# Optimization experiments

Measured on AMD Instinct MI355X. Metric: run time of the kernel, lower is better.

## Reference

```python
import jax, jax.numpy as jnp
import numpy as np

B, S, H = 1, 2048, 2048
NH, KVH = 32, 8
HD = H // NH
GROUPS = NH // KVH
ROPE_THETA = 10000.0


def _rope(x):
    # x: (b, s, heads, head_dim); HF-style rotate-half RoPE
    d = x.shape[-1]
    s = x.shape[1]
    inv_freq = 1.0 / (ROPE_THETA ** (jnp.arange(0, d, 2, dtype=jnp.float32) / d))
    t = jnp.arange(s, dtype=jnp.float32)
    freqs = jnp.einsum('s,f->sf', t, inv_freq)          # (s, d/2)
    emb = jnp.concatenate([freqs, freqs], axis=-1)       # (s, d)
    cos = jnp.cos(emb)[None, :, None, :].astype(x.dtype)
    sin = jnp.sin(emb)[None, :, None, :].astype(x.dtype)
    x1, x2 = x[..., : d // 2], x[..., d // 2:]
    rot = jnp.concatenate([-x2, x1], axis=-1)
    return x * cos + rot * sin


def setup_inputs() -> dict:
    key = jax.random.key(0)
    ks = jax.random.split(key, 6)
    scale = 0.02
    hidden_states = jax.random.normal(ks[0], (B, S, H), dtype=jnp.float32)
    Wq = jax.random.normal(ks[1], (H, NH, HD), dtype=jnp.float32) * scale
    Wk = jax.random.normal(ks[2], (H, KVH, HD), dtype=jnp.float32) * scale
    Wv = jax.random.normal(ks[3], (H, KVH, HD), dtype=jnp.float32) * scale
    Wo = jax.random.normal(ks[4], (H, H), dtype=jnp.float32) * scale
    # causal additive mask (b,1,s,s): 0 on/below diagonal, large negative above
    causal = jnp.tril(jnp.ones((S, S), dtype=bool))
    attention_mask = jnp.where(causal, 0.0, -1e9).astype(jnp.float32)[None, None]
    return {"hidden_states": hidden_states, "Wq": Wq, "Wk": Wk, "Wv": Wv,
            "Wo": Wo, "attention_mask": attention_mask}


def reference(hidden_states, Wq, Wk, Wv, Wo, attention_mask):
    b, s, _ = hidden_states.shape
    q = jnp.einsum('bsh,hnd->bsnd', hidden_states, Wq)   # (b,s,NH,HD)
    k = jnp.einsum('bsh,hnd->bsnd', hidden_states, Wk)   # (b,s,KVH,HD)
    v = jnp.einsum('bsh,hnd->bsnd', hidden_states, Wv)   # (b,s,KVH,HD)
    q = _rope(q)
    k = _rope(k)
    # GQA: tile kv heads along head axis (tf.tile semantics)
    k = jnp.tile(k, (1, 1, GROUPS, 1))                   # (b,s,NH,HD)
    v = jnp.tile(v, (1, 1, GROUPS, 1))
    # scores: 'aecd,abcd->acbe' -> (b, heads, q_len, k_len)
    scores = jnp.einsum('bend,bqnd->bnqe', k, q) / jnp.sqrt(
        jnp.asarray(HD, dtype=q.dtype))
    scores = scores + attention_mask
    scores = jnp.maximum(scores, jnp.finfo(scores.dtype).min)
    probs = jax.nn.softmax(scores, axis=-1)
    attn = jnp.einsum('bnqe,bend->bqnd', probs, v)       # (b,s,NH,HD)
    attn = attn.reshape(b, s, H)
    return jnp.einsum('bsh,hd->bsd', attn, Wo)
```

## Files before the change

kernel.cpp:

```cpp
#include <hip/hip_runtime.h>
#include <stdint.h>

typedef unsigned short u16;
typedef uint32_t u32;
typedef uint64_t u64;
typedef float f32x4 __attribute__((ext_vector_type(4)));
typedef float f32x16 __attribute__((ext_vector_type(16)));
typedef __bf16 bf16x8 __attribute__((ext_vector_type(8)));

#define S_LEN 2048
#define HID 2048
#define N_HEADS 32
#define KV_HEADS 8
#define HEAD_DIM 64
#define QKV_COLS 3072
#define QSCALE 0.18033688011112042f

__device__ __forceinline__ u16 f2b(float x) {
  union { float f; uint32_t u; } c; c.f = x;
  uint32_t u = (c.u + 0x7fffu + ((c.u >> 16) & 1u)) >> 16;
  return (u16)u;
}
__device__ __forceinline__ float b2f(u16 v) {
  union { uint32_t u; float f; } c; c.u = ((uint32_t)v) << 16;
  return c.f;
}
__device__ __forceinline__ u32 pkbf(float e, float o) {
  union { float f; u32 u; } a, b; a.f = e; b.f = o;
  return __builtin_amdgcn_perm(b.u, a.u, 0x07060302u);
}

#define GLL16(gptr, lptr)                                                      \
  __builtin_amdgcn_global_load_lds(                                            \
      (__attribute__((address_space(1))) void*)(gptr),                         \
      (__attribute__((address_space(3))) void*)(lptr), 16, 0, 0)

__global__ __launch_bounds__(256) void prep_fused(const float* __restrict__ Wq,
                                                  const float* __restrict__ Wk,
                                                  const float* __restrict__ Wv,
                                                  const float* __restrict__ Wo,
                                                  const float* __restrict__ hs,
                                                  u16* __restrict__ WqkvT,
                                                  u16* __restrict__ WoT,
                                                  u16* __restrict__ X) {
  const int b = blockIdx.x;
  const int t = threadIdx.x;
  if (b < 10240) {
    __shared__ float tile[32][33];
    const float* in;
    u16* out;
    int C, bx, by;
    if (b < 4096) { in = Wq; out = WqkvT; C = 2048; bx = b & 63; by = b >> 6; }
    else if (b < 5120) { int bb = b - 4096; in = Wk; out = WqkvT + 2048 * 2048; C = 512; bx = bb & 15; by = bb >> 4; }
    else if (b < 6144) { int bb = b - 5120; in = Wv; out = WqkvT + 2048 * 2048 + 512 * 2048; C = 512; bx = bb & 15; by = bb >> 4; }
    else { int bb = b - 6144; in = Wo; out = WoT; C = 2048; bx = bb & 63; by = bb >> 6; }
    const int tx = t & 31, ty = t >> 5;
    const int c0 = bx * 32, r0 = by * 32;
#pragma unroll
    for (int i = 0; i < 32; i += 8)
      tile[ty + i][tx] = in[(size_t)(r0 + ty + i) * C + c0 + tx];
    __syncthreads();
#pragma unroll
    for (int i = 0; i < 32; i += 8)
      out[(size_t)(c0 + ty + i) * 2048 + r0 + tx] = f2b(tile[tx][ty + i]);
  } else {
    int i = (b - 10240) * 256 + t;
    float4 v = reinterpret_cast<const float4*>(hs)[i];
    ushort4 o;
    o.x = f2b(v.x); o.y = f2b(v.y); o.z = f2b(v.z); o.w = f2b(v.w);
    reinterpret_cast<ushort4*>(X)[i] = o;
  }
}

__global__ void transpose_bf16(const u16* __restrict__ in, int istride,
                               u16* __restrict__ out, int R, int C) {
  __shared__ u16 tile[32][33];
  int c0 = blockIdx.x * 32, r0 = blockIdx.y * 32;
  int tx = threadIdx.x, ty = threadIdx.y;
#pragma unroll
  for (int i = 0; i < 32; i += 8)
    tile[ty + i][tx] = in[(size_t)(r0 + ty + i) * istride + c0 + tx];
  __syncthreads();
#pragma unroll
  for (int i = 0; i < 32; i += 8)
    out[(size_t)(c0 + ty + i) * R + r0 + tx] = tile[tx][ty + i];
}

__global__ __launch_bounds__(256) void gemm128s(const u16* __restrict__ A,
                                                const u16* __restrict__ BT,
                                                float* __restrict__ Cp,
                                                int M, int N, int K, int ksplit) {
  __shared__ __align__(16) u16 As[128 * 64];
  __shared__ __align__(16) u16 Bs[128 * 64];
  const int t = threadIdx.x;
  const int w = t >> 6, l = t & 63;
  const int lr = l & 15, lk = l >> 4;
  const int wr = w >> 1, wc = w & 1;
  const int m0 = blockIdx.x * 128, n0 = blockIdx.y * 128;
  const int z = blockIdx.z;
  const int kspan = K / ksplit;
  const int kBeg = z * kspan, kEnd = kBeg + kspan;
  Cp += (size_t)z * M * N;

  f32x4 acc[4][4];
#pragma unroll
  for (int m = 0; m < 4; ++m)
#pragma unroll
    for (int n = 0; n < 4; ++n)
      acc[m][n] = (f32x4){0.f, 0.f, 0.f, 0.f};

  const u16* aSrc = A + (size_t)(m0 + t / 8) * K + (t % 8) * 8;
  const u16* bSrc = BT + (size_t)(n0 + t / 8) * K + (t % 8) * 8;
  char* aDst = (char*)As + w * 1024;
  char* bDst = (char*)Bs + w * 1024;

  for (int k0 = kBeg; k0 < kEnd; k0 += 64) {
#pragma unroll
    for (int i = 0; i < 4; ++i)
      GLL16(aSrc + (size_t)i * 32 * K + k0, aDst + i * 4096);
#pragma unroll
    for (int i = 0; i < 4; ++i)
      GLL16(bSrc + (size_t)i * 32 * K + k0, bDst + i * 4096);
    __syncthreads();
#pragma unroll
    for (int kk = 0; kk < 2; ++kk) {
      bf16x8 af[4], bfr[4];
#pragma unroll
      for (int m = 0; m < 4; ++m)
        af[m] = *(const bf16x8*)&As[(wr * 64 + m * 16 + lr) * 64 + kk * 32 + lk * 8];
#pragma unroll
      for (int n = 0; n < 4; ++n)
        bfr[n] = *(const bf16x8*)&Bs[(wc * 64 + n * 16 + lr) * 64 + kk * 32 + lk * 8];
#pragma unroll
      for (int m = 0; m < 4; ++m)
#pragma unroll
        for (int n = 0; n < 4; ++n)
          acc[m][n] = __builtin_amdgcn_mfma_f32_16x16x32_bf16(af[m], bfr[n], acc[m][n], 0, 0, 0);
    }
    __syncthreads();
  }
#pragma unroll
  for (int m = 0; m < 4; ++m)
#pragma unroll
    for (int n = 0; n < 4; ++n) {
      int row0 = m0 + wr * 64 + m * 16 + lk * 4;
      int col = n0 + wc * 64 + n * 16 + lr;
#pragma unroll
      for (int r = 0; r < 4; ++r)
        Cp[(size_t)(row0 + r) * N + col] = acc[m][n][r];
    }
}

__global__ __launch_bounds__(256) void post_qkv(const float* __restrict__ P0,
                                                const float* __restrict__ P1,
                                                u16* __restrict__ QKV) {
  int idx = blockIdx.x * 256 + threadIdx.x;
  int s = idx / 1536, j = idx - s * 1536;
  const float* r0 = P0 + (size_t)s * QKV_COLS;
  const float* r1 = P1 + (size_t)s * QKV_COLS;
  u16* o = QKV + (size_t)s * QKV_COLS;
  if (j < 1280) {
    int hbase, i;
    float scale;
    if (j < 1024) { hbase = (j >> 5) * 64; i = j & 31; scale = QSCALE; }
    else { int jj = j - 1024; hbase = 2048 + (jj >> 5) * 64; i = jj & 31; scale = 1.0f; }
    int c1 = hbase + i, c2 = c1 + 32;
    float inv = __expf(-(float)i * (9.210340371976184f / 32.0f));
    float f = (float)s * inv;
    float sn, cs;
    sincosf(f, &sn, &cs);
    float x1 = r0[c1] + r1[c1], x2 = r0[c2] + r1[c2];
    o[c1] = f2b((x1 * cs - x2 * sn) * scale);
    o[c2] = f2b((x2 * cs + x1 * sn) * scale);
  } else {
    int c = 2560 + (j - 1280) * 2;
    *(u32*)(o + c) = pkbf(r0[c] + r1[c], r0[c + 1] + r1[c + 1]);
  }
}

__global__ __launch_bounds__(256) void post_out(const float* __restrict__ P0,
                                                const float* __restrict__ P1,
                                                float* __restrict__ out) {
  int i = blockIdx.x * 256 + threadIdx.x;
  float4 a = reinterpret_cast<const float4*>(P0)[i];
  float4 b = reinterpret_cast<const float4*>(P1)[i];
  a.x += b.x; a.y += b.y; a.z += b.z; a.w += b.w;
  reinterpret_cast<float4*>(out)[i] = a;
}

__global__ __launch_bounds__(256) void attn_kernel(const u16* __restrict__ QKV,
                                                   const u16* __restrict__ Vt,
                                                   u16* __restrict__ At) {
  __shared__ __align__(16) u16 scratch[4][32 * 64];
  const int t = threadIdx.x;
  const int w = t >> 6, l = t & 63;
  const int lq = l & 31;
  const int hi = l >> 5;
  const int b = blockIdx.x;
  const int qt = (b < 256) ? (63 - (b >> 3)) : ((b - 256) >> 3);
  const int head = (b & 7) * 4 + w;
  const int kvh = head & (KV_HEADS - 1);
  const int qbase = qt * 32;
  char* pb = (char*)scratch[w];
  const int swrow = lq * 128;
  const int swx = (lq & 7) << 4;

  bf16x8 qf[4];
  {
    const u16* qp = QKV + (size_t)(qbase + lq) * QKV_COLS + head * HEAD_DIM + hi * 8;
#pragma unroll
    for (int jj = 0; jj < 4; ++jj) qf[jj] = *(const bf16x8*)(qp + jj * 16);
  }
  const u16* Kb = QKV + HID + kvh * HEAD_DIM;
  const u16* Vb = Vt + (size_t)(kvh * HEAD_DIM) * S_LEN;

  f32x16 oacc0, oacc1;
#pragma unroll
  for (int i = 0; i < 16; ++i) { oacc0[i] = 0.f; oacc1[i] = 0.f; }
  float m_run = -1e30f;
  float l_run = 0.f;

  auto loadK = [&](int kv0, bf16x8* k0, bf16x8* k1) {
    const u16* kp = Kb + (size_t)(kv0 + lq) * QKV_COLS + hi * 8;
#pragma unroll
    for (int jj = 0; jj < 4; ++jj) {
      k0[jj] = *(const bf16x8*)(kp + jj * 16);
      k1[jj] = *(const bf16x8*)(kp + (size_t)32 * QKV_COLS + jj * 16);
    }
  };

  auto tile = [&](int kv0, const bf16x8* kf0, const bf16x8* kf1, bool mask0, bool mask1) {
    f32x16 s0, s1;
#pragma unroll
    for (int i = 0; i < 16; ++i) { s0[i] = 0.f; s1[i] = 0.f; }
#pragma unroll
    for (int jj = 0; jj < 4; ++jj)
      s0 = __builtin_amdgcn_mfma_f32_32x32x16_bf16(kf0[jj], qf[jj], s0, 0, 0, 0);
#pragma unroll
    for (int jj = 0; jj < 4; ++jj)
      s1 = __builtin_amdgcn_mfma_f32_32x32x16_bf16(kf1[jj], qf[jj], s1, 0, 0, 0);
    bf16x8 vf0[4], vf1[4];
    const u16* vp = Vb + (size_t)lq * S_LEN + kv0 + hi * 8;
#pragma unroll
    for (int ks = 0; ks < 4; ++ks) {
      vf0[ks] = *(const bf16x8*)(vp + ks * 16);
      vf1[ks] = *(const bf16x8*)(vp + (size_t)32 * S_LEN + ks * 16);
    }
    if (mask0) {
      const int c = kv0 - qbase;
#pragma unroll
      for (int r = 0; r < 16; ++r) {
        int kvr = (r & 3) + 8 * (r >> 2) + 4 * hi + c;
        s0[r] = (kvr > lq) ? -1e30f : s0[r];
      }
    }
    if (mask1) {
      const int c = kv0 + 32 - qbase;
#pragma unroll
      for (int r = 0; r < 16; ++r) {
        int kvr = (r & 3) + 8 * (r >> 2) + 4 * hi + c;
        s1[r] = (kvr > lq) ? -1e30f : s1[r];
      }
    }
    float mx[16];
#pragma unroll
    for (int r = 0; r < 16; ++r) mx[r] = fmaxf(s0[r], s1[r]);
#pragma unroll
    for (int st = 8; st >= 1; st >>= 1)
#pragma unroll
      for (int r = 0; r < st; ++r) mx[r] = fmaxf(mx[r], mx[r + st]);
    float pm = mx[0];
    pm = fmaxf(pm, __shfl_xor(pm, 32));
    if (!__all(pm <= m_run + 8.f)) {
      float mnew = fmaxf(m_run, pm);
      float esc = exp2f(m_run - mnew);
      m_run = mnew;
      l_run *= esc;
#pragma unroll
      for (int i = 0; i < 16; ++i) { oacc0[i] *= esc; oacc1[i] *= esc; }
    }
#pragma unroll
    for (int r = 0; r < 16; ++r) {
      s0[r] = exp2f(s0[r] - m_run);
      s1[r] = exp2f(s1[r] - m_run);
    }
    float ls[16];
#pragma unroll
    for (int r = 0; r < 16; ++r) ls[r] = s0[r] + s1[r];
#pragma unroll
    for (int st = 8; st >= 1; st >>= 1)
#pragma unroll
      for (int r = 0; r < st; ++r) ls[r] += ls[r + st];
    l_run += ls[0];
#pragma unroll
    for (int sb = 0; sb < 2; ++sb)
#pragma unroll
      for (int g = 0; g < 4; ++g) {
        u32 w0 = sb ? pkbf(s1[4 * g + 0], s1[4 * g + 1]) : pkbf(s0[4 * g + 0], s0[4 * g + 1]);
        u32 w1 = sb ? pkbf(s1[4 * g + 2], s1[4 * g + 3]) : pkbf(s0[4 * g + 2], s0[4 * g + 3]);
        int kvb2 = (32 * sb + 8 * g + 4 * hi) * 2;
        *(u64*)(pb + swrow + (kvb2 ^ swx)) = (u64)w0 | ((u64)w1 << 32);
      }
    asm volatile("s_waitcnt lgkmcnt(0)" ::: "memory");
    __builtin_amdgcn_sched_barrier(0);
    bf16x8 pa[4];
#pragma unroll
    for (int ks = 0; ks < 4; ++ks)
      pa[ks] = *(const bf16x8*)(pb + swrow + ((32 * ks + 16 * hi) ^ swx));
    asm volatile("" ::: "memory");
#pragma unroll
    for (int ks = 0; ks < 4; ++ks) {
      oacc0 = __builtin_amdgcn_mfma_f32_32x32x16_bf16(vf0[ks], pa[ks], oacc0, 0, 0, 0);
      oacc1 = __builtin_amdgcn_mfma_f32_32x32x16_bf16(vf1[ks], pa[ks], oacc1, 0, 0, 0);
    }
  };

  const int NTF = qt >> 1;
  bf16x8 ka0[4], ka1[4], kb0[4], kb1[4];
  loadK(0, ka0, ka1);
  int tl = 0;
  for (; tl + 2 <= NTF; tl += 2) {
    loadK((tl + 1) * 64, kb0, kb1);
    tile(tl * 64, ka0, ka1, false, false);
    loadK((tl + 2) * 64, ka0, ka1);
    tile((tl + 1) * 64, kb0, kb1, false, false);
  }
  if (tl < NTF) {
    loadK((tl + 1) * 64, kb0, kb1);
    tile(tl * 64, ka0, ka1, false, false);
    tile(NTF * 64, kb0, kb1, (qt & 1) == 0, true);
  } else {
    tile(NTF * 64, ka0, ka1, (qt & 1) == 0, true);
  }

  float l_tot = l_run + __shfl_xor(l_run, 32);
  float inv = 1.0f / l_tot;
  asm volatile("" ::: "memory");
#pragma unroll
  for (int dt = 0; dt < 2; ++dt) {
#pragma unroll
    for (int j = 0; j < 8; ++j) {
      int d = dt * 32 + 2 * (j & 1) + 8 * (j >> 1) + 4 * hi;
      float e = (dt ? oacc1[2 * j] : oacc0[2 * j]) * inv;
      float o = (dt ? oacc1[2 * j + 1] : oacc0[2 * j + 1]) * inv;
      *(u32*)(pb + swrow + ((d * 2) ^ swx)) = pkbf(e, o);
    }
  }
  asm volatile("s_waitcnt lgkmcnt(0)" ::: "memory");
  __builtin_amdgcn_sched_barrier(0);
#pragma unroll
  for (int pass = 0; pass < 4; ++pass) {
    int qq = pass * 8 + (l >> 3);
    int coff = (l & 7) * 16;
    f32x4 v = *(const f32x4*)(pb + qq * 128 + (coff ^ ((qq & 7) << 4)));
    *(f32x4*)&At[(size_t)(qbase + qq) * HID + head * HEAD_DIM + (l & 7) * 8] = v;
  }
}

extern "C" void kernel_launch(void* const* d_in, const int* in_sizes, int n_in,
                              void* d_out, int out_size, void* d_ws, size_t ws_size,
                              hipStream_t stream) {
  const float* hs = (const float*)d_in[0];
  const float* Wq = (const float*)d_in[1];
  const float* Wk = (const float*)d_in[2];
  const float* Wv = (const float*)d_in[3];
  const float* Wo = (const float*)d_in[4];

  char* ws = (char*)d_ws;
  const size_t MB = 1024 * 1024;
  u16* X      = (u16*)(ws + 0 * MB);
  u16* WqkvT  = (u16*)(ws + 8 * MB);
  u16* WoT    = (u16*)(ws + 20 * MB);
  u16* QKV    = (u16*)(ws + 28 * MB);
  u16* Vt     = (u16*)(ws + 40 * MB);
  u16* At     = (u16*)(ws + 42 * MB);
  float* QKVp = (float*)(ws + 50 * MB);
  float* Op   = (float*)(ws + 50 * MB);

  prep_fused<<<14336, 256, 0, stream>>>(Wq, Wk, Wv, Wo, hs, WqkvT, WoT, X);
  gemm128s<<<dim3(16, 24, 2), 256, 0, stream>>>(X, WqkvT, QKVp, 2048, QKV_COLS, 2048, 2);
  post_qkv<<<12288, 256, 0, stream>>>(QKVp, QKVp + (size_t)2048 * QKV_COLS, QKV);
  transpose_bf16<<<dim3(16, 64), dim3(32, 8), 0, stream>>>(QKV + HID + 512, QKV_COLS, Vt, 2048, 512);
  attn_kernel<<<dim3(512), 256, 0, stream>>>(QKV, Vt, At);
  gemm128s<<<dim3(16, 16, 2), 256, 0, stream>>>(At, WoT, Op, 2048, 2048, 2048, 2);
  post_out<<<4096, 256, 0, stream>>>(Op, Op + (size_t)2048 * 2048, (float*)d_out);
}
```

Measured before the change: 293.0 us.

## Fuse RoPE into QKV GEMM epilogue, drop split-K, share K/V tiles in attention

Replaces the split-K 128x128 GEMMs and their separate reduction kernels with a 64x128 tile GEMM that writes final results. The QKV GEMM epilogue applies RoPE from a precomputed cos/sin table built in the prep kernel. The output GEMM writes fp32 straight to the output buffer. Attention is reorganized so the four waves of a block share one KV head, with K/V tiles double-buffered in LDS via global_load_lds instead of per-wave direct loads. This removes the partial-sum round trips and extra launches, at the cost of a block-wide sync per KV tile and a longer serial K loop per block.

```diff
diff --git a/kernel.cpp b/kernel.cpp
--- a/kernel.cpp
+++ b/kernel.cpp
@@ -10,7 +10,6 @@
 
 #define S_LEN 2048
 #define HID 2048
-#define N_HEADS 32
 #define KV_HEADS 8
 #define HEAD_DIM 64
 #define QKV_COLS 3072
@@ -20,10 +19,6 @@
   union { float f; uint32_t u; } c; c.f = x;
   uint32_t u = (c.u + 0x7fffu + ((c.u >> 16) & 1u)) >> 16;
   return (u16)u;
-}
-__device__ __forceinline__ float b2f(u16 v) {
-  union { uint32_t u; float f; } c; c.u = ((uint32_t)v) << 16;
-  return c.f;
 }
 __device__ __forceinline__ u32 pkbf(float e, float o) {
   union { float f; u32 u; } a, b; a.f = e; b.f = o;
@@ -42,7 +37,8 @@
                                                   const float* __restrict__ hs,
                                                   u16* __restrict__ WqkvT,
                                                   u16* __restrict__ WoT,
-                                                  u16* __restrict__ X) {
+                                                  u16* __restrict__ X,
+                                                  float2* __restrict__ tbl) {
   const int b = blockIdx.x;
   const int t = threadIdx.x;
   if (b < 10240) {
@@ -63,12 +59,20 @@
 #pragma unroll
     for (int i = 0; i < 32; i += 8)
       out[(size_t)(c0 + ty + i) * 2048 + r0 + tx] = f2b(tile[tx][ty + i]);
-  } else {
+  } else if (b < 14336) {
     int i = (b - 10240) * 256 + t;
     float4 v = reinterpret_cast<const float4*>(hs)[i];
     ushort4 o;
     o.x = f2b(v.x); o.y = f2b(v.y); o.z = f2b(v.z); o.w = f2b(v.w);
     reinterpret_cast<ushort4*>(X)[i] = o;
+  } else {
+    int idx = (b - 14336) * 256 + t;
+    int s = idx >> 5, i = idx & 31;
+    float inv = __expf(-(float)i * 0.28782313662425572f);
+    float f = (float)s * inv;
+    float sn, cs;
+    sincosf(f, &sn, &cs);
+    tbl[idx] = make_float2(cs, sn);
   }
 }
 
@@ -86,25 +90,23 @@
     out[(size_t)(c0 + ty + i) * R + r0 + tx] = tile[tx][ty + i];
 }
 
-__global__ __launch_bounds__(256) void gemm128s(const u16* __restrict__ A,
-                                                const u16* __restrict__ BT,
-                                                float* __restrict__ Cp,
-                                                int M, int N, int K, int ksplit) {
-  __shared__ __align__(16) u16 As[128 * 64];
+template <int MODE>
+__global__ __launch_bounds__(256) void gemm64(const u16* __restrict__ A,
+                                              const u16* __restrict__ BT,
+                                              void* __restrict__ Cp,
+                                              const float2* __restrict__ tbl,
+                                              int M, int N, int K) {
+  __shared__ __align__(16) u16 As[64 * 64];
   __shared__ __align__(16) u16 Bs[128 * 64];
   const int t = threadIdx.x;
   const int w = t >> 6, l = t & 63;
   const int lr = l & 15, lk = l >> 4;
   const int wr = w >> 1, wc = w & 1;
-  const int m0 = blockIdx.x * 128, n0 = blockIdx.y * 128;
-  const int z = blockIdx.z;
-  const int kspan = K / ksplit;
-  const int kBeg = z * kspan, kEnd = kBeg + kspan;
-  Cp += (size_t)z * M * N;
-
-  f32x4 acc[4][4];
-#pragma unroll
-  for (int m = 0; m < 4; ++m)
+  const int m0 = blockIdx.x * 64, n0 = blockIdx.y * 128;
+
+  f32x4 acc[2][4];
+#pragma unroll
+  for (int m = 0; m < 2; ++m)
 #pragma unroll
     for (int n = 0; n < 4; ++n)
       acc[m][n] = (f32x4){0.f, 0.f, 0.f, 0.f};
@@ -114,9 +116,9 @@
   char* aDst = (char*)As + w * 1024;
   char* bDst = (char*)Bs + w * 1024;
 
-  for (int k0 = kBeg; k0 < kEnd; k0 += 64) {
-#pragma unroll
-    for (int i = 0; i < 4; ++i)
+  for (int k0 = 0; k0 < K; k0 += 64) {
+#pragma unroll
+    for (int i = 0; i < 2; ++i)
       GLL16(aSrc + (size_t)i * 32 * K + k0, aDst + i * 4096);
 #pragma unroll
     for (int i = 0; i < 4; ++i)
@@ -124,86 +126,85 @@
     __syncthreads();
 #pragma unroll
     for (int kk = 0; kk < 2; ++kk) {
-      bf16x8 af[4], bfr[4];
-#pragma unroll
-      for (int m = 0; m < 4; ++m)
-        af[m] = *(const bf16x8*)&As[(wr * 64 + m * 16 + lr) * 64 + kk * 32 + lk * 8];
+      bf16x8 af[2], bfr[4];
+#pragma unroll
+      for (int m = 0; m < 2; ++m)
+        af[m] = *(const bf16x8*)&As[(wr * 32 + m * 16 + lr) * 64 + kk * 32 + lk * 8];
 #pragma unroll
       for (int n = 0; n < 4; ++n)
         bfr[n] = *(const bf16x8*)&Bs[(wc * 64 + n * 16 + lr) * 64 + kk * 32 + lk * 8];
 #pragma unroll
-      for (int m = 0; m < 4; ++m)
+      for (int m = 0; m < 2; ++m)
 #pragma unroll
         for (int n = 0; n < 4; ++n)
           acc[m][n] = __builtin_amdgcn_mfma_f32_16x16x32_bf16(af[m], bfr[n], acc[m][n], 0, 0, 0);
     }
     __syncthreads();
   }
-#pragma unroll
-  for (int m = 0; m < 4; ++m)
-#pragma unroll
-    for (int n = 0; n < 4; ++n) {
-      int row0 = m0 + wr * 64 + m * 16 + lk * 4;
-      int col = n0 + wc * 64 + n * 16 + lr;
-#pragma unroll
-      for (int r = 0; r < 4; ++r)
-        Cp[(size_t)(row0 + r) * N + col] = acc[m][n][r];
-    }
-}
-
-__global__ __launch_bounds__(256) void post_qkv(const float* __restrict__ P0,
-                                                const float* __restrict__ P1,
-                                                u16* __restrict__ QKV) {
-  int idx = blockIdx.x * 256 + threadIdx.x;
-  int s = idx / 1536, j = idx - s * 1536;
-  const float* r0 = P0 + (size_t)s * QKV_COLS;
-  const float* r1 = P1 + (size_t)s * QKV_COLS;
-  u16* o = QKV + (size_t)s * QKV_COLS;
-  if (j < 1280) {
-    int hbase, i;
-    float scale;
-    if (j < 1024) { hbase = (j >> 5) * 64; i = j & 31; scale = QSCALE; }
-    else { int jj = j - 1024; hbase = 2048 + (jj >> 5) * 64; i = jj & 31; scale = 1.0f; }
-    int c1 = hbase + i, c2 = c1 + 32;
-    float inv = __expf(-(float)i * (9.210340371976184f / 32.0f));
-    float f = (float)s * inv;
-    float sn, cs;
-    sincosf(f, &sn, &cs);
-    float x1 = r0[c1] + r1[c1], x2 = r0[c2] + r1[c2];
-    o[c1] = f2b((x1 * cs - x2 * sn) * scale);
-    o[c2] = f2b((x2 * cs + x1 * sn) * scale);
+  if constexpr (MODE == 0) {
+    float* C = (float*)Cp;
+#pragma unroll
+    for (int m = 0; m < 2; ++m)
+#pragma unroll
+      for (int n = 0; n < 4; ++n) {
+        int row0 = m0 + wr * 32 + m * 16 + lk * 4;
+        int col = n0 + wc * 64 + n * 16 + lr;
+#pragma unroll
+        for (int r = 0; r < 4; ++r)
+          C[(size_t)(row0 + r) * N + col] = acc[m][n][r];
+      }
   } else {
-    int c = 2560 + (j - 1280) * 2;
-    *(u32*)(o + c) = pkbf(r0[c] + r1[c], r0[c + 1] + r1[c + 1]);
-  }
-}
-
-__global__ __launch_bounds__(256) void post_out(const float* __restrict__ P0,
-                                                const float* __restrict__ P1,
-                                                float* __restrict__ out) {
-  int i = blockIdx.x * 256 + threadIdx.x;
-  float4 a = reinterpret_cast<const float4*>(P0)[i];
-  float4 b = reinterpret_cast<const float4*>(P1)[i];
-  a.x += b.x; a.y += b.y; a.z += b.z; a.w += b.w;
-  reinterpret_cast<float4*>(out)[i] = a;
+    u16* C = (u16*)Cp;
+#pragma unroll
+    for (int m = 0; m < 2; ++m)
+#pragma unroll
+      for (int n = 0; n < 2; ++n) {
+        int col1 = n0 + wc * 64 + n * 16 + lr;
+        int row0 = m0 + wr * 32 + m * 16 + lk * 4;
+        if (col1 >= 2560) {
+#pragma unroll
+          for (int r = 0; r < 4; ++r) {
+            C[(size_t)(row0 + r) * N + col1] = f2b(acc[m][n][r]);
+            C[(size_t)(row0 + r) * N + col1 + 32] = f2b(acc[m][n + 2][r]);
+          }
+        } else {
+          float sc = (col1 < 2048) ? QSCALE : 1.0f;
+          int pos = n * 16 + lr;
+#pragma unroll
+          for (int r = 0; r < 4; ++r) {
+            float2 cs = tbl[(row0 + r) * 32 + pos];
+            float x1 = acc[m][n][r], x2 = acc[m][n + 2][r];
+            C[(size_t)(row0 + r) * N + col1] = f2b((x1 * cs.x - x2 * cs.y) * sc);
+            C[(size_t)(row0 + r) * N + col1 + 32] = f2b((x2 * cs.x + x1 * cs.y) * sc);
+          }
+        }
+      }
+  }
 }
 
 __global__ __launch_bounds__(256) void attn_kernel(const u16* __restrict__ QKV,
                                                    const u16* __restrict__ Vt,
                                                    u16* __restrict__ At) {
-  __shared__ __align__(16) u16 scratch[4][32 * 64];
+  __shared__ __align__(16) u16 Kl[2][64 * 64];
+  __shared__ __align__(16) u16 Vl[2][64 * 64];
+  __shared__ __align__(16) char Pl[4][4096];
   const int t = threadIdx.x;
   const int w = t >> 6, l = t & 63;
-  const int lq = l & 31;
-  const int hi = l >> 5;
+  const int lq = l & 31, hi = l >> 5;
   const int b = blockIdx.x;
-  const int qt = (b < 256) ? (63 - (b >> 3)) : ((b - 256) >> 3);
-  const int head = (b & 7) * 4 + w;
-  const int kvh = head & (KV_HEADS - 1);
+  const int pb = b >> 1;
+  const int kvh = pb & 7, qh = pb >> 3;
+  const int qt = (b & 1) ? qh : 63 - qh;
+  const int head = kvh + w * 8;
   const int qbase = qt * 32;
-  char* pb = (char*)scratch[w];
+  char* pw = Pl[w];
   const int swrow = lq * 128;
   const int swx = (lq & 7) << 4;
+
+  const int srow = l >> 3;
+  const int gx = (l & 7) ^ srow;
+  const u16* Ksrc = QKV + HID + kvh * HEAD_DIM + gx * 8;
+  const u16* Vsrc = Vt + (size_t)(kvh * HEAD_DIM) * S_LEN + gx * 8;
 
   bf16x8 qf[4];
   {
@@ -211,8 +212,6 @@
 #pragma unroll
     for (int jj = 0; jj < 4; ++jj) qf[jj] = *(const bf16x8*)(qp + jj * 16);
   }
-  const u16* Kb = QKV + HID + kvh * HEAD_DIM;
-  const u16* Vb = Vt + (size_t)(kvh * HEAD_DIM) * S_LEN;
 
   f32x16 oacc0, oacc1;
 #pragma unroll
@@ -220,16 +219,36 @@
   float m_run = -1e30f;
   float l_run = 0.f;
 
-  auto loadK = [&](int kv0, bf16x8* k0, bf16x8* k1) {
-    const u16* kp = Kb + (size_t)(kv0 + lq) * QKV_COLS + hi * 8;
+  auto STAGE = [&](int buf, int kv0) {
+#pragma unroll
+    for (int i = 0; i < 2; ++i) {
+      int row = w * 16 + i * 8 + srow;
+      GLL16(Ksrc + (size_t)(kv0 + row) * QKV_COLS, (char*)Kl[buf] + (w * 16 + i * 8) * 128);
+      GLL16(Vsrc + (size_t)row * S_LEN + kv0, (char*)Vl[buf] + (w * 16 + i * 8) * 128);
+    }
+  };
+
+  const int NT = (qt >> 1) + 1;
+  STAGE(0, 0);
+  asm volatile("s_waitcnt vmcnt(0)" ::: "memory");
+  __syncthreads();
+
+  for (int j = 0; j < NT; ++j) {
+    const int cur = j & 1;
+    if (j + 1 < NT) STAGE(cur ^ 1, (j + 1) * 64);
+    const int kv0 = j * 64;
+    const bool tail = (j == NT - 1);
+    const bool mask0 = tail && ((qt & 1) == 0);
+    const bool mask1 = tail;
+    const char* KB = (const char*)Kl[cur];
+    const char* VB = (const char*)Vl[cur];
+    bf16x8 kf0[4], kf1[4];
 #pragma unroll
     for (int jj = 0; jj < 4; ++jj) {
-      k0[jj] = *(const bf16x8*)(kp + jj * 16);
-      k1[jj] = *(const bf16x8*)(kp + (size_t)32 * QKV_COLS + jj * 16);
-    }
-  };
-
-  auto tile = [&](int kv0, const bf16x8* kf0, const bf16x8* kf1, bool mask0, bool mask1) {
+      int off = (hi * 16 + jj * 32) ^ swx;
+      kf0[jj] = *(const bf16x8*)(KB + swrow + off);
+      kf1[jj] = *(const bf16x8*)(KB + swrow + 32 * 128 + off);
+    }
     f32x16 s0, s1;
 #pragma unroll
     for (int i = 0; i < 16; ++i) { s0[i] = 0.f; s1[i] = 0.f; }
@@ -240,11 +259,11 @@
     for (int jj = 0; jj < 4; ++jj)
       s1 = __builtin_amdgcn_mfma_f32_32x32x16_bf16(kf1[jj], qf[jj], s1, 0, 0, 0);
     bf16x8 vf0[4], vf1[4];
-    const u16* vp = Vb + (size_t)lq * S_LEN + kv0 + hi * 8;
 #pragma unroll
     for (int ks = 0; ks < 4; ++ks) {
-      vf0[ks] = *(const bf16x8*)(vp + ks * 16);
-      vf1[ks] = *(const bf16x8*)(vp + (size_t)32 * S_LEN + ks * 16);
+      int off = (ks * 32 + hi * 16) ^ swx;
+      vf0[ks] = *(const bf16x8*)(VB + swrow + off);
+      vf1[ks] = *(const bf16x8*)(VB + swrow + 32 * 128 + off);
     }
     if (mask0) {
       const int c = kv0 - qbase;
@@ -299,38 +318,22 @@
         u32 w0 = sb ? pkbf(s1[4 * g + 0], s1[4 * g + 1]) : pkbf(s0[4 * g + 0], s0[4 * g + 1]);
         u32 w1 = sb ? pkbf(s1[4 * g + 2], s1[4 * g + 3]) : pkbf(s0[4 * g + 2], s0[4 * g + 3]);
         int kvb2 = (32 * sb + 8 * g + 4 * hi) * 2;
-        *(u64*)(pb + swrow + (kvb2 ^ swx)) = (u64)w0 | ((u64)w1 << 32);
+        *(u64*)(pw + swrow + (kvb2 ^ swx)) = (u64)w0 | ((u64)w1 << 32);
       }
     asm volatile("s_waitcnt lgkmcnt(0)" ::: "memory");
     __builtin_amdgcn_sched_barrier(0);
     bf16x8 pa[4];
 #pragma unroll
     for (int ks = 0; ks < 4; ++ks)
-      pa[ks] = *(const bf16x8*)(pb + swrow + ((32 * ks + 16 * hi) ^ swx));
+      pa[ks] = *(const bf16x8*)(pw + swrow + ((32 * ks + 16 * hi) ^ swx));
     asm volatile("" ::: "memory");
 #pragma unroll
     for (int ks = 0; ks < 4; ++ks) {
       oacc0 = __builtin_amdgcn_mfma_f32_32x32x16_bf16(vf0[ks], pa[ks], oacc0, 0, 0, 0);
       oacc1 = __builtin_amdgcn_mfma_f32_32x32x16_bf16(vf1[ks], pa[ks], oacc1, 0, 0, 0);
     }
-  };
-
-  const int NTF = qt >> 1;
-  bf16x8 ka0[4], ka1[4], kb0[4], kb1[4];
-  loadK(0, ka0, ka1);
-  int tl = 0;
-  for (; tl + 2 <= NTF; tl += 2) {
-    loadK((tl + 1) * 64, kb0, kb1);
-    tile(tl * 64, ka0, ka1, false, false);
-    loadK((tl + 2) * 64, ka0, ka1);
-    tile((tl + 1) * 64, kb0, kb1, false, false);
-  }
-  if (tl < NTF) {
-    loadK((tl + 1) * 64, kb0, kb1);
-    tile(tl * 64, ka0, ka1, false, false);
-    tile(NTF * 64, kb0, kb1, (qt & 1) == 0, true);
-  } else {
-    tile(NTF * 64, ka0, ka1, (qt & 1) == 0, true);
+    asm volatile("s_waitcnt vmcnt(0)" ::: "memory");
+    __syncthreads();
   }
 
   float l_tot = l_run + __shfl_xor(l_run, 32);
@@ -343,7 +346,7 @@
       int d = dt * 32 + 2 * (j & 1) + 8 * (j >> 1) + 4 * hi;
       float e = (dt ? oacc1[2 * j] : oacc0[2 * j]) * inv;
       float o = (dt ? oacc1[2 * j + 1] : oacc0[2 * j + 1]) * inv;
-      *(u32*)(pb + swrow + ((d * 2) ^ swx)) = pkbf(e, o);
+      *(u32*)(pw + swrow + ((d * 2) ^ swx)) = pkbf(e, o);
     }
   }
   asm volatile("s_waitcnt lgkmcnt(0)" ::: "memory");
@@ -352,7 +355,7 @@
   for (int pass = 0; pass < 4; ++pass) {
     int qq = pass * 8 + (l >> 3);
     int coff = (l & 7) * 16;
-    f32x4 v = *(const f32x4*)(pb + qq * 128 + (coff ^ ((qq & 7) << 4)));
+    f32x4 v = *(const f32x4*)(pw + qq * 128 + (coff ^ ((qq & 7) << 4)));
     *(f32x4*)&At[(size_t)(qbase + qq) * HID + head * HEAD_DIM + (l & 7) * 8] = v;
   }
 }
@@ -374,14 +377,11 @@
   u16* QKV    = (u16*)(ws + 28 * MB);
   u16* Vt     = (u16*)(ws + 40 * MB);
   u16* At     = (u16*)(ws + 42 * MB);
-  float* QKVp = (float*)(ws + 50 * MB);
-  float* Op   = (float*)(ws + 50 * MB);
-
-  prep_fused<<<14336, 256, 0, stream>>>(Wq, Wk, Wv, Wo, hs, WqkvT, WoT, X);
-  gemm128s<<<dim3(16, 24, 2), 256, 0, stream>>>(X, WqkvT, QKVp, 2048, QKV_COLS, 2048, 2);
-  post_qkv<<<12288, 256, 0, stream>>>(QKVp, QKVp + (size_t)2048 * QKV_COLS, QKV);
+  float2* TBL = (float2*)(ws + 50 * MB);
+
+  prep_fused<<<14592, 256, 0, stream>>>(Wq, Wk, Wv, Wo, hs, WqkvT, WoT, X, TBL);
+  gemm64<1><<<dim3(32, 24), 256, 0, stream>>>(X, WqkvT, QKV, TBL, 2048, QKV_COLS, 2048);
   transpose_bf16<<<dim3(16, 64), dim3(32, 8), 0, stream>>>(QKV + HID + 512, QKV_COLS, Vt, 2048, 512);
-  attn_kernel<<<dim3(512), 256, 0, stream>>>(QKV, Vt, At);
-  gemm128s<<<dim3(16, 16, 2), 256, 0, stream>>>(At, WoT, Op, 2048, 2048, 2048, 2);
-  post_out<<<4096, 256, 0, stream>>>(Op, Op + (size_t)2048 * 2048, (float*)d_out);
-}
+  attn_kernel<<<512, 256, 0, stream>>>(QKV, Vt, At);
+  gemm64<0><<<dim3(32, 16), 256, 0, stream>>>(At, WoT, d_out, nullptr, 2048, 2048, 2048);
+}
```

Result: faster. 254.6 us (-13.1%).
